# Performance work log

Hardware: AMD Instinct MI355X
Metric: run time of the kernel (lower is better)

The kernel has to match this reference:

```python
import jax, jax.numpy as jnp
import numpy as np

B, D, L = 16, 64, 2048
NUM_TOKENS = 8192


def setup_inputs() -> dict:
    key = jax.random.key(0)
    k1, k2 = jax.random.split(key)
    z_e = jax.random.normal(k1, (B, D, L), dtype=jnp.float32)
    codebook = jax.random.normal(k2, (NUM_TOKENS, D), dtype=jnp.float32)
    return {"z_e": z_e, "codebook": codebook}


def reference(z_e, codebook):
    # z_e: [B, D, L] -> per-position vectors [B, L, D]
    x = jnp.transpose(z_e, (0, 2, 1))          # [B, L, D]
    xf = x.reshape(-1, x.shape[-1])            # [N, D], N = B*L
    x2 = jnp.sum(xf * xf, axis=-1, keepdims=True)            # [N, 1]
    c2 = jnp.sum(codebook * codebook, axis=-1)               # [K]
    d2 = x2 - 2.0 * (xf @ codebook.T) + c2[None, :]          # [N, K]
    idx = jnp.argmin(d2, axis=-1)                            # [N]
    zq = codebook[idx]                                        # [N, D] gather
    zq = zq.reshape(x.shape)                                  # [B, L, D]
    # straight-through with codebook stop-gradient (code_sg=True)
    zq_st = x + jax.lax.stop_gradient(zq - x)                 # [B, L, D]
    v_q = jnp.transpose(zq_st, (0, 2, 1))                     # [B, D, L]
    indices = idx.reshape(z_e.shape[0], -1)                   # [B, L]
    return v_q, indices
```

## Files before the change

kernel.cpp:

```cpp
#include <hip/hip_runtime.h>
#include <cstdint>

#define BB 16
#define DD 64
#define LL 2048
#define NQ (BB*LL)
#define KK 8192
#define VQ_SIZE (BB*DD*LL)
#define CHUNK 256
#define NCH (KK/CHUNK)
#define QSL 256
#define QPS (NQ/QSL)
#define MARGIN 0.75f

typedef __attribute__((ext_vector_type(8))) short short8;
typedef __attribute__((ext_vector_type(4))) float f32x4;
typedef unsigned long long u64;


static __device__ inline short f2bf(float f) {
    uint32_t u = __float_as_uint(f);
    uint32_t r = (u + 0x7FFFu + ((u >> 16) & 1u)) >> 16;
    return (short)r;
}

__global__ __launch_bounds__(256) void prep_x(const float* __restrict__ ze,
                                              short* __restrict__ xb) {
    __shared__ float t[64][65];
    const int b = blockIdx.x;
    const int l0 = blockIdx.y * 64;
    const int tid = threadIdx.x;
    #pragma unroll
    for (int it = 0; it < 4; ++it) {
        int id = it * 256 + tid;
        int d = id >> 4;
        int lw = (id & 15) * 4;
        const float4 v = *(const float4*)(ze + ((size_t)b * DD + d) * LL + l0 + lw);
        t[d][lw + 0] = v.x; t[d][lw + 1] = v.y; t[d][lw + 2] = v.z; t[d][lw + 3] = v.w;
    }
    __syncthreads();
    #pragma unroll
    for (int it = 0; it < 2; ++it) {
        int id = it * 256 + tid;
        int lr = id >> 3;
        int u = id & 7;
        short8 o;
        #pragma unroll
        for (int e = 0; e < 8; ++e) o[e] = f2bf(t[u * 8 + e][lr]);
        *(short8*)(xb + (size_t)(b * LL + l0 + lr) * DD + u * 8) = o;
    }
}

__global__ __launch_bounds__(256) void prep_xf(const float* __restrict__ ze,
                                               float* __restrict__ xf) {
    __shared__ float t[64][65];
    const int b = blockIdx.x;
    const int l0 = blockIdx.y * 64;
    const int tid = threadIdx.x;
    #pragma unroll
    for (int it = 0; it < 4; ++it) {
        int id = it * 256 + tid;
        int d = id >> 4;
        int lw = (id & 15) * 4;
        const float4 v = *(const float4*)(ze + ((size_t)b * DD + d) * LL + l0 + lw);
        t[d][lw + 0] = v.x; t[d][lw + 1] = v.y; t[d][lw + 2] = v.z; t[d][lw + 3] = v.w;
    }
    __syncthreads();
    #pragma unroll
    for (int it = 0; it < 4; ++it) {
        int id = it * 256 + tid;
        int row = id >> 4;
        int u = id & 15;
        float4 o = make_float4(t[4 * u + 0][row], t[4 * u + 1][row],
                               t[4 * u + 2][row], t[4 * u + 3][row]);
        *(float4*)(xf + (size_t)(b * LL + l0 + row) * DD + u * 4) = o;
    }
}

__global__ __launch_bounds__(256) void prep_nh2(const float* __restrict__ cbf,
                                                float* __restrict__ nh2) {
    int k = blockIdx.x * 256 + threadIdx.x;
    const float4* c4 = (const float4*)(cbf + (size_t)k * DD);
    float s = 0.f;
    #pragma unroll
    for (int i = 0; i < DD / 4; ++i) {
        float4 v = c4[i];
        s += v.x * v.x + v.y * v.y + v.z * v.z + v.w * v.w;
    }
    nh2[k] = -0.5f * s;
}

__global__ __launch_bounds__(256) void vq_screen(const float* __restrict__ cbf,
                                                 const float* __restrict__ nh2,
                                                 const short* __restrict__ xb,
                                                 float* __restrict__ cmaxT) {
    __shared__ short cbt[CHUNK * 64];
    __shared__ float sh2[CHUNK];
    const int tid = threadIdx.x;
    const int lane = tid & 63;
    const int wid = tid >> 6;
    const int kbase = blockIdx.y * CHUNK;
    const int qbase = blockIdx.x * 256 + wid * 64;
    const int r16 = lane & 15, g = lane >> 4;

    #pragma unroll
    for (int it = 0; it < 8; ++it) {
        int id = it * 256 + tid;
        int row = id >> 3;
        int u = id & 7;
        const float4 lo = *(const float4*)(cbf + (size_t)(kbase + row) * 64 + u * 8);
        const float4 hi = *(const float4*)(cbf + (size_t)(kbase + row) * 64 + u * 8 + 4);
        short8 o;
        o[0] = f2bf(lo.x); o[1] = f2bf(lo.y); o[2] = f2bf(lo.z); o[3] = f2bf(lo.w);
        o[4] = f2bf(hi.x); o[5] = f2bf(hi.y); o[6] = f2bf(hi.z); o[7] = f2bf(hi.w);
        *(short8*)(&cbt[row * 64 + ((u ^ (row & 7)) * 8)]) = o;
    }
    sh2[tid] = nh2[kbase + tid];
    __syncthreads();

    short8 a[4][2];
    #pragma unroll
    for (int t = 0; t < 4; ++t)
        #pragma unroll
        for (int ks = 0; ks < 2; ++ks)
            a[t][ks] = *(const short8*)(xb + (size_t)(qbase + t * 16 + r16) * 64 + ks * 32 + g * 8);

    float rm[4][4];
    #pragma unroll
    for (int t = 0; t < 4; ++t)
        #pragma unroll
        for (int j = 0; j < 4; ++j) rm[t][j] = -3.4e38f;

    for (int cs = 0; cs < CHUNK / 16; ++cs) {
        const int rowb = cs * 16 + r16;
        const float nh = sh2[rowb];
        const f32x4 ci = {nh, nh, nh, nh};
        const short8 b0 = *(const short8*)(&cbt[rowb * 64 + ((g ^ (rowb & 7)) * 8)]);
        const short8 b1 = *(const short8*)(&cbt[rowb * 64 + (((g + 4) ^ (rowb & 7)) * 8)]);
        #pragma unroll
        for (int t = 0; t < 4; ++t) {
            f32x4 acc = __builtin_amdgcn_mfma_f32_16x16x32_bf16(a[t][0], b0, ci, 0, 0, 0);
            acc = __builtin_amdgcn_mfma_f32_16x16x32_bf16(a[t][1], b1, acc, 0, 0, 0);
            rm[t][0] = fmaxf(rm[t][0], acc[0]);
            rm[t][1] = fmaxf(rm[t][1], acc[1]);
            rm[t][2] = fmaxf(rm[t][2], acc[2]);
            rm[t][3] = fmaxf(rm[t][3], acc[3]);
        }
    }

    #pragma unroll
    for (int s = 1; s < 16; s <<= 1)
        #pragma unroll
        for (int t = 0; t < 4; ++t)
            #pragma unroll
            for (int j = 0; j < 4; ++j)
                rm[t][j] = fmaxf(rm[t][j], __shfl_xor(rm[t][j], s));

    if (r16 == 0) {
        #pragma unroll
        for (int t = 0; t < 4; ++t)
            #pragma unroll
            for (int j = 0; j < 4; ++j)
                cmaxT[(size_t)blockIdx.y * NQ + (qbase + t * 16 + g * 4 + j)] = rm[t][j];
    }
}

__global__ __launch_bounds__(256) void vq_cand(const float* __restrict__ cmaxT,
                                               u64* __restrict__ qmask,
                                               u64* __restrict__ keys) {
    const int tid = threadIdx.x;
    const int lane = tid & 63;
    const int q = blockIdx.x * 256 + tid;
    const int qword = q >> 6;
    float v[NCH];
    float m = -3.4e38f;
    #pragma unroll
    for (int j = 0; j < NCH; ++j) {
        v[j] = cmaxT[(size_t)j * NQ + q];
        m = fmaxf(m, v[j]);
    }
    keys[q] = ~0ULL;
    const float thr = m - MARGIN;
    #pragma unroll
    for (int j = 0; j < NCH; ++j) {
        u64 mm = __ballot(v[j] >= thr);
        if (lane == 0) qmask[(size_t)j * (NQ / 64) + qword] = mm;
    }
}

__global__ __launch_bounds__(256) void vq_exact(const float* __restrict__ xf,
                                                const float* __restrict__ cbf,
                                                const float* __restrict__ nh2,
                                                const u64* __restrict__ qmask,
                                                u64* __restrict__ keys) {
    const int ch = blockIdx.x;
    const int slice = blockIdx.y;
    const int lane = threadIdx.x & 63;
    const int wid = threadIdx.x >> 6;
    const int kb = ch * CHUNK + wid * 64;
    const int k = kb + lane;

    const u64* wm = qmask + (size_t)ch * (NQ / 64) + slice * (QPS / 64);
    u64 words[QPS / 64];
    u64 any = 0;
    #pragma unroll
    for (int w = 0; w < QPS / 64; ++w) {
        u64 x = wm[w];
        uint32_t lo = __builtin_amdgcn_readfirstlane((uint32_t)x);
        uint32_t hi = __builtin_amdgcn_readfirstlane((uint32_t)(x >> 32));
        words[w] = ((u64)hi << 32) | lo;
        any |= words[w];
    }
    if (!any) return;

    float cdv[64];
    #pragma unroll
    for (int i = 0; i < 16; ++i)
        *(float4*)&cdv[4 * i] = *(const float4*)(cbf + (size_t)k * DD + 4 * i);
    const float nh2k = nh2[k];

    #pragma unroll 1
    for (int w = 0; w < QPS / 64; ++w) {
        u64 sw = words[w];
        while (sw) {
            const int bit = __ffsll((long long)sw) - 1;
            sw &= sw - 1;
            const int q = slice * QPS + w * 64 + bit;
            const float4* xr4 = (const float4*)(xf + (size_t)q * DD);
            float4 xv[16];
            #pragma unroll
            for (int i = 0; i < 16; ++i) xv[i] = xr4[i];

            float a0 = 0.f, a1 = 0.f, a2 = 0.f, a3 = 0.f;
            #pragma unroll
            for (int i = 0; i < 16; ++i) {
                a0 = fmaf(xv[i].x, cdv[4 * i + 0], a0);
                a1 = fmaf(xv[i].y, cdv[4 * i + 1], a1);
                a2 = fmaf(xv[i].z, cdv[4 * i + 2], a2);
                a3 = fmaf(xv[i].w, cdv[4 * i + 3], a3);
            }
            float val = -(((a0 + a1) + (a2 + a3)) + nh2k);

            float mn = val;
            #pragma unroll
            for (int s = 1; s < 64; s <<= 1) mn = fminf(mn, __shfl_xor(mn, s));
            u64 mk = __ballot(val == mn);
            int srcl = __ffsll((long long)mk) - 1;
            uint32_t uu = __float_as_uint(mn);
            uint32_t ub = ((int)uu < 0) ? ~uu : (uu | 0x80000000u);
            u64 key = ((u64)ub << 32) | (unsigned)(kb + srcl);
            if (lane == 0) atomicMin(&keys[q], key);
        }
    }
}

__global__ __launch_bounds__(256) void vq_gather(const float* __restrict__ cb,
                                                 const u64* __restrict__ keys,
                                                 float* __restrict__ vq,
                                                 float* __restrict__ oidx) {
    int t = blockIdx.x * 256 + threadIdx.x;
    int l = t & (LL - 1);
    int bd = t >> 11;
    int d = bd & 63;
    int b = bd >> 6;
    int idx = (int)(unsigned)(keys[b * LL + l] & 0x1FFFu);
    vq[t] = cb[idx * DD + d];
    if (d == 0) oidx[b * LL + l] = (float)idx;
}

extern "C" void kernel_launch(void* const* d_in, const int* in_sizes, int n_in,
                              void* d_out, int out_size, void* d_ws, size_t ws_size,
                              hipStream_t stream) {
    const float* ze = (const float*)d_in[0];
    const float* cb = (const float*)d_in[1];
    float* out = (float*)d_out;

    short* xb = (short*)d_out;
    float* cmaxT = (float*)((char*)d_out + (size_t)NQ * DD * 2);
    float* xf = (float*)d_out;
    u64* qmask = (u64*)(out + VQ_SIZE);
    float* nh2 = (float*)d_ws;
    u64* keys = (u64*)((char*)d_ws + (size_t)KK * 4);
    float* oidx = out + VQ_SIZE;

    dim3 gx(BB, LL / 64);
    prep_x<<<gx, 256, 0, stream>>>(ze, xb);
    prep_nh2<<<KK / 256, 256, 0, stream>>>(cb, nh2);

    dim3 gs(NQ / 256, NCH);
    vq_screen<<<gs, 256, 0, stream>>>(cb, nh2, xb, cmaxT);

    vq_cand<<<NQ / 256, 256, 0, stream>>>(cmaxT, qmask, keys);

    prep_xf<<<gx, 256, 0, stream>>>(ze, xf);

    dim3 ge(NCH, QSL);
    vq_exact<<<ge, 256, 0, stream>>>(xf, cb, nh2, qmask, keys);

    vq_gather<<<VQ_SIZE / 256, 256, 0, stream>>>(cb, keys, out, oidx);
}
```

Before: 165.6 us.

## Use one mask word per exact-check block and DPP wave min-reduction

Doubles the number of query slices so each vq_exact block handles exactly one 64-bit candidate mask word, removing the per-block word loop and raising the number of blocks. It also replaces the shuffle-based wave minimum with DPP row_shr/row_bcast fmin steps plus a readlane of lane 63. Together these aim to spread sparse rescoring work across more blocks and cut reduction latency. The cost is more blocks that each reload a codebook row into registers, and the DPP sequence relies on correct bank and row masks.

Result: slower. 203.1 us (+22.7%).

```diff
diff --git a/kernel.cpp b/kernel.cpp
--- a/kernel.cpp
+++ b/kernel.cpp
@@ -9,7 +9,7 @@
 #define VQ_SIZE (BB*DD*LL)
 #define CHUNK 256
 #define NCH (KK/CHUNK)
-#define QSL 256
+#define QSL 512
 #define QPS (NQ/QSL)
 #define MARGIN 0.75f
 
@@ -23,6 +23,13 @@
     uint32_t r = (u + 0x7FFFu + ((u >> 16) & 1u)) >> 16;
     return (short)r;
 }
+
+#define FMIN_DPP(v, ctrl)                                                     \
+    do {                                                                      \
+        int _vi = __float_as_int(v);                                          \
+        int _sh = __builtin_amdgcn_update_dpp(_vi, _vi, (ctrl), 0xf, 0xf, false); \
+        (v) = fminf((v), __int_as_float(_sh));                                \
+    } while (0)
 
 __global__ __launch_bounds__(256) void prep_x(const float* __restrict__ ze,
                                               short* __restrict__ xb) {
@@ -200,18 +207,11 @@
     const int kb = ch * CHUNK + wid * 64;
     const int k = kb + lane;
 
-    const u64* wm = qmask + (size_t)ch * (NQ / 64) + slice * (QPS / 64);
-    u64 words[QPS / 64];
-    u64 any = 0;
-    #pragma unroll
-    for (int w = 0; w < QPS / 64; ++w) {
-        u64 x = wm[w];
-        uint32_t lo = __builtin_amdgcn_readfirstlane((uint32_t)x);
-        uint32_t hi = __builtin_amdgcn_readfirstlane((uint32_t)(x >> 32));
-        words[w] = ((u64)hi << 32) | lo;
-        any |= words[w];
-    }
-    if (!any) return;
+    u64 x = qmask[(size_t)ch * (NQ / 64) + slice];
+    uint32_t lo = __builtin_amdgcn_readfirstlane((uint32_t)x);
+    uint32_t hi = __builtin_amdgcn_readfirstlane((uint32_t)(x >> 32));
+    u64 sw = ((u64)hi << 32) | lo;
+    if (!sw) return;
 
     float cdv[64];
     #pragma unroll
@@ -219,38 +219,41 @@
         *(float4*)&cdv[4 * i] = *(const float4*)(cbf + (size_t)k * DD + 4 * i);
     const float nh2k = nh2[k];
 
-    #pragma unroll 1
-    for (int w = 0; w < QPS / 64; ++w) {
-        u64 sw = words[w];
-        while (sw) {
-            const int bit = __ffsll((long long)sw) - 1;
-            sw &= sw - 1;
-            const int q = slice * QPS + w * 64 + bit;
-            const float4* xr4 = (const float4*)(xf + (size_t)q * DD);
-            float4 xv[16];
-            #pragma unroll
-            for (int i = 0; i < 16; ++i) xv[i] = xr4[i];
-
-            float a0 = 0.f, a1 = 0.f, a2 = 0.f, a3 = 0.f;
-            #pragma unroll
-            for (int i = 0; i < 16; ++i) {
-                a0 = fmaf(xv[i].x, cdv[4 * i + 0], a0);
-                a1 = fmaf(xv[i].y, cdv[4 * i + 1], a1);
-                a2 = fmaf(xv[i].z, cdv[4 * i + 2], a2);
-                a3 = fmaf(xv[i].w, cdv[4 * i + 3], a3);
-            }
-            float val = -(((a0 + a1) + (a2 + a3)) + nh2k);
-
-            float mn = val;
-            #pragma unroll
-            for (int s = 1; s < 64; s <<= 1) mn = fminf(mn, __shfl_xor(mn, s));
-            u64 mk = __ballot(val == mn);
-            int srcl = __ffsll((long long)mk) - 1;
-            uint32_t uu = __float_as_uint(mn);
-            uint32_t ub = ((int)uu < 0) ? ~uu : (uu | 0x80000000u);
-            u64 key = ((u64)ub << 32) | (unsigned)(kb + srcl);
-            if (lane == 0) atomicMin(&keys[q], key);
+    while (sw) {
+        const int bit = __ffsll((long long)sw) - 1;
+        sw &= sw - 1;
+        const int q = slice * QPS + bit;
+        const float4* xr4 = (const float4*)(xf + (size_t)q * DD);
+        float4 xv[16];
+        #pragma unroll
+        for (int i = 0; i < 16; ++i) xv[i] = xr4[i];
+
+        float a0 = 0.f, a1 = 0.f, a2 = 0.f, a3 = 0.f;
+        #pragma unroll
+        for (int i = 0; i < 16; ++i) {
+            a0 = fmaf(xv[i].x, cdv[4 * i + 0], a0);
+            a1 = fmaf(xv[i].y, cdv[4 * i + 1], a1);
+            a2 = fmaf(xv[i].z, cdv[4 * i + 2], a2);
+            a3 = fmaf(xv[i].w, cdv[4 * i + 3], a3);
         }
+        float val = -(((a0 + a1) + (a2 + a3)) + nh2k);
+
+        float mn = val;
+        FMIN_DPP(mn, 0x111);
+        FMIN_DPP(mn, 0x112);
+        FMIN_DPP(mn, 0x114);
+        FMIN_DPP(mn, 0x118);
+        FMIN_DPP(mn, 0x142);
+        FMIN_DPP(mn, 0x143);
+        const float mnall = __uint_as_float(
+            __builtin_amdgcn_readlane(__float_as_uint(mn), 63));
+
+        u64 mk = __ballot(val == mnall);
+        int srcl = __ffsll((long long)mk) - 1;
+        uint32_t uu = __float_as_uint(mnall);
+        uint32_t ub = ((int)uu < 0) ? ~uu : (uu | 0x80000000u);
+        u64 key = ((u64)ub << 32) | (unsigned)(kb + srcl);
+        if (lane == 0) atomicMin(&keys[q], key);
     }
 }
 
```
